# Kernel optimization log

Measured on AMD Instinct MI355X. Metric: run time of the kernel, lower is better.

## Reference

```python
import jax, jax.numpy as jnp
import numpy as np

K_BINS = 8192
HIDDEN = 2048
SQRT2 = 1.4142135623730951
LEAKY_SLOPE = 0.01
TMIN = 1e-10


def setup_inputs() -> dict:
    key = jax.random.key(0)
    k0, k1, k2 = jax.random.split(key, 3)
    D = 2 * K_BINS  # mu length so that cat([mu, t]) has 2K+1 features
    # positive mu keeps mu ** (gamma - 1/(1-gamma)) (a fractional power) finite
    mu = jax.random.uniform(k0, (D,), jnp.float32, 0.1, 1.0)
    t = jnp.array([0.5], jnp.float32)
    gamma = jnp.array([0.5], jnp.float32)  # 1/(1-gamma) = 2 -> integral exponent
    W1 = jax.random.normal(k1, (D + 1, HIDDEN), jnp.float32) * (1.0 / np.sqrt(D + 1))
    b1 = jnp.zeros((HIDDEN,), jnp.float32)
    W2 = jax.random.normal(k2, (HIDDEN, D), jnp.float32) * (1.0 / np.sqrt(HIDDEN))
    b2 = jnp.zeros((D,), jnp.float32)
    return {"mu": mu, "t": t, "gamma": gamma, "W1": W1, "b1": b1,
            "W2": W2, "b2": b2, "K": K_BINS}


def reference(mu, t, gamma, W1, b1, W2, b2, K):
    g = gamma[0]
    # --- NN(cat([mu, t])) -> (mu_epsilon, ln_sigma_epsilon), each [K] ---
    inp = jnp.concatenate([mu, t])                      # [2K+1]
    h = jax.nn.leaky_relu(inp @ W1 + b1, LEAKY_SLOPE)   # [hidden]
    out = h @ W2 + b2                                   # [2K]
    mu_eps, ln_sig = out[:K], out[K:]
    # --- mu_x / sigma_x (t < tmin branch folded in via where) ---
    p_mu = g - 1.0 / (1.0 - g)
    p_eps = 1.0 / (1.0 - g)
    mu_x_nn = jnp.power(mu[:K], p_mu) * jnp.power(mu_eps, p_eps)
    sigma_x_nn = jnp.power(1.0 - g, -0.5) * jnp.exp(0.5 * ln_sig)
    use_nn = t[0] >= TMIN
    mu_x = jnp.where(use_nn, mu_x_nn, jnp.zeros_like(mu_eps))     # [K]
    sigma_x = jnp.where(use_nn, sigma_x_nn, jnp.ones_like(mu_eps))  # [K]
    # --- vectorized discretised CDF differences over the (D_out, K) grid ---
    kk = jnp.arange(K, dtype=jnp.float32)
    kl = 2.0 * (kk - 1.0) / (K - 1.0)   # left bin edges  [K]
    kr = 2.0 * kk / (K - 1.0)           # right bin edges [K]

    def cdf(x):  # x: [K] edges -> G: [D_out, K]
        z = (x[None, :] - mu_x[:, None]) / (sigma_x[:, None] * SQRT2)
        F = 0.5 * (1.0 + jax.lax.erf(z))
        return jnp.where(x[None, :] <= -1.0, 0.0,
                         jnp.where(x[None, :] >= 1.0, 1.0, F))

    return cdf(kr) - cdf(kl)  # [K, K] per-bin probabilities
```

## Files before the change

kernel.cpp:

```cpp
#include <hip/hip_runtime.h>
#include <math.h>

#define KBINS 8192
#define DDIM  16384
#define HID   2048
#define NROWS1 16385

#define C1 32
#define R1P 513
#define C2 32
#define R2P 64

static constexpr float SQRT2_F = 1.4142135623730951f;

__device__ __forceinline__ float fast_erff(float x) {
    float ax = fabsf(x);
    float t  = 1.0f / fmaf(0.3275911f, ax, 1.0f);
    float p  = t * (0.254829592f +
               t * (-0.284496736f +
               t * (1.421413741f +
               t * (-1.453152027f +
               t * 1.061405429f))));
    float r = 1.0f - p * __expf(-ax * ax);
    return copysignf(r, x);
}

__global__ void __launch_bounds__(256)
mv1_partial(const float* __restrict__ mu, const float* __restrict__ t,
            const float* __restrict__ W1, float* __restrict__ part) {
    __shared__ float a_s[C1];
    int r0 = blockIdx.y * C1;
    int nr = NROWS1 - r0; if (nr > C1) nr = C1;
    if (threadIdx.x < C1) {
        int r = r0 + threadIdx.x;
        float a = 0.f;
        if (threadIdx.x < nr) a = (r < DDIM) ? mu[r] : t[0];
        a_s[threadIdx.x] = a;
    }
    __syncthreads();
    int c0 = (blockIdx.x * 256 + threadIdx.x) * 4;
    float4 acc = {0.f, 0.f, 0.f, 0.f};
    for (int k = 0; k < nr; ++k) {
        float a = a_s[k];
        const float4 w = *reinterpret_cast<const float4*>(W1 + (size_t)(r0 + k) * HID + c0);
        acc.x += a * w.x; acc.y += a * w.y; acc.z += a * w.z; acc.w += a * w.w;
    }
    *reinterpret_cast<float4*>(part + (size_t)blockIdx.y * HID + c0) = acc;
}

__global__ void __launch_bounds__(256)
mv2_fused(const float* __restrict__ part1, const float* __restrict__ b1,
          const float* __restrict__ W2, float* __restrict__ part2) {
    __shared__ float red[8][C1];
    __shared__ float hs[C1];
    int r0 = blockIdx.y * C2;
    int part = threadIdx.x >> 5;
    int hidx = threadIdx.x & 31;
    float s = 0.f;
    for (int rb = part; rb < R1P; rb += 8)
        s += part1[(size_t)rb * HID + r0 + hidx];
    red[part][hidx] = s;
    __syncthreads();
    if (threadIdx.x < C1) {
        float v = b1[r0 + threadIdx.x];
        for (int p = 0; p < 8; ++p) v += red[p][threadIdx.x];
        hs[threadIdx.x] = (v >= 0.f) ? v : 0.01f * v;
    }
    __syncthreads();
    int c0 = (blockIdx.x * 256 + threadIdx.x) * 4;
    float4 acc = {0.f, 0.f, 0.f, 0.f};
    for (int k = 0; k < C2; ++k) {
        float a = hs[k];
        const float4 w = *reinterpret_cast<const float4*>(W2 + (size_t)(r0 + k) * DDIM + c0);
        acc.x += a * w.x; acc.y += a * w.y; acc.z += a * w.z; acc.w += a * w.w;
    }
    *reinterpret_cast<float4*>(part2 + (size_t)blockIdx.y * DDIM + c0) = acc;
}

__global__ void __launch_bounds__(256)
cdf_fused(const float* __restrict__ part2, const float* __restrict__ b2,
          const float* __restrict__ mu, const float* __restrict__ t,
          const float* __restrict__ gamma, float* __restrict__ out) {
    int i   = blockIdx.x;
    int tid = threadIdx.x;
    __shared__ float sh[2];
    if (tid < 128) {
        int which = tid >> 6;
        int lane  = tid & 63;
        float v = part2[(size_t)lane * DDIM + i + which * KBINS];
        for (int off = 32; off; off >>= 1) v += __shfl_xor(v, off, 64);
        if (lane == 0) sh[which] = v + b2[i + which * KBINS];
    }
    __syncthreads();
    float g  = gamma[0];
    float pe = 1.0f / (1.0f - g);
    float pm = g - pe;
    bool use_nn = (t[0] >= 1e-10f);
    float s0 = sh[0], s1 = sh[1];
    float m   = use_nn ? powf(mu[i], pm) * powf(s0, pe)       : 0.0f;
    float sx  = use_nn ? powf(1.0f - g, -0.5f) * expf(0.5f * s1) : 1.0f;
    float inv = 1.0f / (sx * SQRT2_F);
    const float sc = 2.0f / 8191.0f;

    float* orow = out + (size_t)i * KBINS;
#pragma unroll
    for (int it = 0; it < 8; ++it) {
        int j0 = it * 1024 + tid * 4;
        float4 r;
        if (j0 > 4096) {
            r.x = r.y = r.z = r.w = 0.f;
        } else {
            float F[5];
#pragma unroll
            for (int k = 0; k < 5; ++k) {
                float x = (float)(j0 - 1 + k) * sc;
                float f;
                if (x >= 1.0f)       f = 1.0f;
                else if (x <= -1.0f) f = 0.0f;
                else                 f = 0.5f * (1.0f + fast_erff((x - m) * inv));
                F[k] = f;
            }
            r.x = F[1] - F[0]; r.y = F[2] - F[1]; r.z = F[3] - F[2]; r.w = F[4] - F[3];
        }
        *reinterpret_cast<float4*>(orow + j0) = r;
    }
}

extern "C" void kernel_launch(void* const* d_in, const int* in_sizes, int n_in,
                              void* d_out, int out_size, void* d_ws, size_t ws_size,
                              hipStream_t stream) {
    const float* mu    = (const float*)d_in[0];
    const float* t     = (const float*)d_in[1];
    const float* gamma = (const float*)d_in[2];
    const float* W1    = (const float*)d_in[3];
    const float* b1    = (const float*)d_in[4];
    const float* W2    = (const float*)d_in[5];
    const float* b2    = (const float*)d_in[6];
    float* out = (float*)d_out;

    float* ws    = (float*)d_ws;
    float* part1 = ws;
    float* part2 = part1 + (size_t)R1P * HID;

    mv1_partial<<<dim3(2, R1P),  dim3(256), 0, stream>>>(mu, t, W1, part1);
    mv2_fused  <<<dim3(16, R2P), dim3(256), 0, stream>>>(part1, b1, W2, part2);
    cdf_fused  <<<dim3(KBINS),   dim3(256), 0, stream>>>(part2, b2, mu, t, gamma, out);
}
```

Before: 165.2 us.

## Split MLP reductions into dedicated kernels and precompute per-row CDF scalars

Measured after the change: 166.2 us. No clear change (+0.6%).

```diff
diff --git a/kernel.cpp b/kernel.cpp
--- a/kernel.cpp
+++ b/kernel.cpp
@@ -4,12 +4,12 @@
 #define KBINS 8192
 #define DDIM  16384
 #define HID   2048
-#define NROWS1 16385
+#define LASTROW 16384
 
 #define C1 32
-#define R1P 513
+#define NB1 512
 #define C2 32
-#define R2P 64
+#define NB2 64
 
 static constexpr float SQRT2_F = 1.4142135623730951f;
 
@@ -26,82 +26,95 @@
 }
 
 __global__ void __launch_bounds__(256)
-mv1_partial(const float* __restrict__ mu, const float* __restrict__ t,
-            const float* __restrict__ W1, float* __restrict__ part) {
+mv1_partial(const float* __restrict__ mu, const float* __restrict__ W1,
+            float* __restrict__ part1) {
     __shared__ float a_s[C1];
     int r0 = blockIdx.y * C1;
-    int nr = NROWS1 - r0; if (nr > C1) nr = C1;
-    if (threadIdx.x < C1) {
-        int r = r0 + threadIdx.x;
-        float a = 0.f;
-        if (threadIdx.x < nr) a = (r < DDIM) ? mu[r] : t[0];
-        a_s[threadIdx.x] = a;
-    }
+    if (threadIdx.x < C1) a_s[threadIdx.x] = mu[r0 + threadIdx.x];
     __syncthreads();
     int c0 = (blockIdx.x * 256 + threadIdx.x) * 4;
     float4 acc = {0.f, 0.f, 0.f, 0.f};
-    for (int k = 0; k < nr; ++k) {
+    const float* wp = W1 + (size_t)r0 * HID + c0;
+#pragma unroll 8
+    for (int k = 0; k < C1; ++k) {
         float a = a_s[k];
-        const float4 w = *reinterpret_cast<const float4*>(W1 + (size_t)(r0 + k) * HID + c0);
+        const float4 w = *reinterpret_cast<const float4*>(wp + (size_t)k * HID);
         acc.x += a * w.x; acc.y += a * w.y; acc.z += a * w.z; acc.w += a * w.w;
     }
-    *reinterpret_cast<float4*>(part + (size_t)blockIdx.y * HID + c0) = acc;
+    *reinterpret_cast<float4*>(part1 + (size_t)blockIdx.y * HID + c0) = acc;
 }
 
 __global__ void __launch_bounds__(256)
-mv2_fused(const float* __restrict__ part1, const float* __restrict__ b1,
-          const float* __restrict__ W2, float* __restrict__ part2) {
-    __shared__ float red[8][C1];
-    __shared__ float hs[C1];
+h_reduce(const float* __restrict__ part1, const float* __restrict__ b1,
+         const float* __restrict__ W1, const float* __restrict__ t,
+         float* __restrict__ h) {
+    __shared__ float red[4][64];
+    int lane = threadIdx.x & 63;
+    int sub  = threadIdx.x >> 6;
+    int col  = blockIdx.x * 64 + lane;
+    float s = 0.f;
+    for (int rb = sub; rb < NB1; rb += 4)
+        s += part1[(size_t)rb * HID + col];
+    red[sub][lane] = s;
+    __syncthreads();
+    if (threadIdx.x < 64) {
+        int c = blockIdx.x * 64 + threadIdx.x;
+        float v = b1[c] + t[0] * W1[(size_t)LASTROW * HID + c];
+        v += red[0][threadIdx.x] + red[1][threadIdx.x]
+           + red[2][threadIdx.x] + red[3][threadIdx.x];
+        h[c] = (v >= 0.f) ? v : 0.01f * v;
+    }
+}
+
+__global__ void __launch_bounds__(256)
+mv2_partial(const float* __restrict__ h, const float* __restrict__ W2,
+            float* __restrict__ part2) {
+    __shared__ float hs[C2];
     int r0 = blockIdx.y * C2;
-    int part = threadIdx.x >> 5;
-    int hidx = threadIdx.x & 31;
-    float s = 0.f;
-    for (int rb = part; rb < R1P; rb += 8)
-        s += part1[(size_t)rb * HID + r0 + hidx];
-    red[part][hidx] = s;
-    __syncthreads();
-    if (threadIdx.x < C1) {
-        float v = b1[r0 + threadIdx.x];
-        for (int p = 0; p < 8; ++p) v += red[p][threadIdx.x];
-        hs[threadIdx.x] = (v >= 0.f) ? v : 0.01f * v;
-    }
+    if (threadIdx.x < C2) hs[threadIdx.x] = h[r0 + threadIdx.x];
     __syncthreads();
     int c0 = (blockIdx.x * 256 + threadIdx.x) * 4;
     float4 acc = {0.f, 0.f, 0.f, 0.f};
+    const float* wp = W2 + (size_t)r0 * DDIM + c0;
+#pragma unroll 8
     for (int k = 0; k < C2; ++k) {
         float a = hs[k];
-        const float4 w = *reinterpret_cast<const float4*>(W2 + (size_t)(r0 + k) * DDIM + c0);
+        const float4 w = *reinterpret_cast<const float4*>(wp + (size_t)k * DDIM);
         acc.x += a * w.x; acc.y += a * w.y; acc.z += a * w.z; acc.w += a * w.w;
     }
     *reinterpret_cast<float4*>(part2 + (size_t)blockIdx.y * DDIM + c0) = acc;
 }
 
 __global__ void __launch_bounds__(256)
-cdf_fused(const float* __restrict__ part2, const float* __restrict__ b2,
-          const float* __restrict__ mu, const float* __restrict__ t,
-          const float* __restrict__ gamma, float* __restrict__ out) {
-    int i   = blockIdx.x;
-    int tid = threadIdx.x;
-    __shared__ float sh[2];
-    if (tid < 128) {
-        int which = tid >> 6;
-        int lane  = tid & 63;
-        float v = part2[(size_t)lane * DDIM + i + which * KBINS];
-        for (int off = 32; off; off >>= 1) v += __shfl_xor(v, off, 64);
-        if (lane == 0) sh[which] = v + b2[i + which * KBINS];
+scalars(const float* __restrict__ part2, const float* __restrict__ b2,
+        const float* __restrict__ mu, const float* __restrict__ t,
+        const float* __restrict__ gamma,
+        float* __restrict__ mu_x, float* __restrict__ sigma_x) {
+    int i = blockIdx.x * 256 + threadIdx.x;
+    float s0 = b2[i];
+    float s1 = b2[i + KBINS];
+    for (int rb = 0; rb < NB2; ++rb) {
+        s0 += part2[(size_t)rb * DDIM + i];
+        s1 += part2[(size_t)rb * DDIM + i + KBINS];
     }
-    __syncthreads();
     float g  = gamma[0];
     float pe = 1.0f / (1.0f - g);
     float pm = g - pe;
     bool use_nn = (t[0] >= 1e-10f);
-    float s0 = sh[0], s1 = sh[1];
-    float m   = use_nn ? powf(mu[i], pm) * powf(s0, pe)       : 0.0f;
-    float sx  = use_nn ? powf(1.0f - g, -0.5f) * expf(0.5f * s1) : 1.0f;
-    float inv = 1.0f / (sx * SQRT2_F);
+    float mx = powf(mu[i], pm) * powf(s0, pe);
+    float sx = powf(1.0f - g, -0.5f) * expf(0.5f * s1);
+    mu_x[i]    = use_nn ? mx : 0.0f;
+    sigma_x[i] = use_nn ? sx : 1.0f;
+}
+
+__global__ void __launch_bounds__(256)
+cdf_row(const float* __restrict__ mu_x, const float* __restrict__ sigma_x,
+        float* __restrict__ out) {
+    int i   = blockIdx.x;
+    int tid = threadIdx.x;
+    float m   = mu_x[i];
+    float inv = 1.0f / (sigma_x[i] * SQRT2_F);
     const float sc = 2.0f / 8191.0f;
-
     float* orow = out + (size_t)i * KBINS;
 #pragma unroll
     for (int it = 0; it < 8; ++it) {
@@ -138,11 +151,16 @@
     const float* b2    = (const float*)d_in[6];
     float* out = (float*)d_out;
 
-    float* ws    = (float*)d_ws;
-    float* part1 = ws;
-    float* part2 = part1 + (size_t)R1P * HID;
+    float* ws      = (float*)d_ws;
+    float* part1   = ws;
+    float* h       = part1 + (size_t)NB1 * HID;
+    float* part2   = h + HID;
+    float* mu_x    = part2 + (size_t)NB2 * DDIM;
+    float* sigma_x = mu_x + KBINS;
 
-    mv1_partial<<<dim3(2, R1P),  dim3(256), 0, stream>>>(mu, t, W1, part1);
-    mv2_fused  <<<dim3(16, R2P), dim3(256), 0, stream>>>(part1, b1, W2, part2);
-    cdf_fused  <<<dim3(KBINS),   dim3(256), 0, stream>>>(part2, b2, mu, t, gamma, out);
+    mv1_partial<<<dim3(2, NB1),  dim3(256), 0, stream>>>(mu, W1, part1);
+    h_reduce   <<<dim3(32),      dim3(256), 0, stream>>>(part1, b1, W1, t, h);
+    mv2_partial<<<dim3(16, NB2), dim3(256), 0, stream>>>(h, W2, part2);
+    scalars    <<<dim3(32),      dim3(256), 0, stream>>>(part2, b2, mu, t, gamma, mu_x, sigma_x);
+    cdf_row    <<<dim3(KBINS),   dim3(256), 0, stream>>>(mu_x, sigma_x, out);
 }
```
